# Kernel tuning notes

Hardware: AMD Instinct MI355X
Metric: run time of the kernel (lower is better)

The kernel has to match this reference:

```python
import jax, jax.numpy as jnp
import numpy as np
from itertools import combinations

F = 24                 # num_fields
VOCAB_PER_FIELD = 10000
D = 16                 # embed_dim
B = 2048               # batch
FIELD_DIMS = [VOCAB_PER_FIELD] * F
TOTAL_VOCAB = sum(FIELD_DIMS)
# FeaturesEmbedding/FeaturesLinear offsets: cumulative field dims
OFFSETS = np.concatenate(([0], np.cumsum(FIELD_DIMS)[:-1])).astype(np.int64)  # (F,)
PAIRS = np.array(list(combinations(range(F), 2)), dtype=np.int64)   # (276, 2)
TRIPS = np.array(list(combinations(range(F), 3)), dtype=np.int64)   # (2024, 3)


def setup_inputs() -> dict:
    key = jax.random.key(0)
    k0, k1, k2, k3, k4 = jax.random.split(key, 5)
    x = jax.random.randint(k0, (B, F), 0, VOCAB_PER_FIELD)
    embed_table = jax.random.normal(k1, (TOTAL_VOCAB, D), dtype=jnp.float32) * 0.01
    lin_weight = jax.random.normal(k2, (TOTAL_VOCAB, 1), dtype=jnp.float32) * 0.01
    lin_bias = jnp.zeros((1,), dtype=jnp.float32)
    genotype_2nd = jax.random.normal(k3, (PAIRS.shape[0], 1), dtype=jnp.float32)
    genotype_3rd = jax.random.normal(k4, (TRIPS.shape[0], 1), dtype=jnp.float32)
    return {
        "x": x,
        "embed_table": embed_table,
        "lin_weight": lin_weight,
        "lin_bias": lin_bias,
        "genotype_2nd": genotype_2nd,
        "genotype_3rd": genotype_3rd,
    }


def reference(x, embed_table, lin_weight, lin_bias, genotype_2nd, genotype_3rd):
    idx = x + jnp.asarray(OFFSETS)[None, :]            # (B, F) global ids
    emb = embed_table[idx]                             # (B, F, D)
    # genotype is detached in the original forward
    g2 = jax.lax.stop_gradient(genotype_2nd)[:, 0]     # (P,)
    g3 = jax.lax.stop_gradient(genotype_3rd)[:, 0]     # (T,)
    # 2nd-order gated interactions: sum_t sum_d g2[t] * e_i * e_j
    p = emb[:, PAIRS[:, 0]]                            # (B, P, D)
    q = emb[:, PAIRS[:, 1]]
    nasfm_2nd = jnp.einsum('bpd,bpd,p->b', p, q, g2)   # (B,)
    # 3rd-order gated interactions
    p1 = emb[:, TRIPS[:, 0]]                           # (B, T, D)
    q1 = emb[:, TRIPS[:, 1]]
    r1 = emb[:, TRIPS[:, 2]]
    nasfm_3rd = jnp.einsum('btd,btd,btd,t->b', p1, q1, r1, g3)  # (B,)
    # FeaturesLinear: sum of per-feature weights + bias
    linear = jnp.sum(lin_weight[idx][..., 0], axis=1) + lin_bias[0]  # (B,)
    return jax.nn.sigmoid(linear + nasfm_2nd + nasfm_3rd)
```

## Files before the change

### kernel.cpp

```cpp
#include <hip/hip_runtime.h>
#include <math.h>

#define F 24
#define D 16
#define BATCH 2048
#define NPAIR 276
#define NTRIP 2024
#define VOCAB 10000
#define SLAB 392
#define LONG_SLOTS 80
#define SHORT_SLOTS 224
#define LONG_F (LONG_SLOTS * 28)
#define CW_FLOATS (LONG_F + SHORT_SLOTS * 16)

__host__ __device__ constexpr int pair_base(int i) { return i * 23 - i * (i - 1) / 2; }
__host__ __device__ constexpr int trip_base(int i) {
    return NTRIP - (24 - i) * (23 - i) * (22 - i) / 6;
}
__host__ __device__ constexpr int trip_idx(int i, int j, int k) {
    return trip_base(i) + (j - i - 1) * (46 - i - j) / 2 + (k - j - 1);
}

__global__ void repack_kernel(const float* __restrict__ g2,
                              const float* __restrict__ g3,
                              float* __restrict__ cw) {
    const int tid = threadIdx.x;
    for (int t = tid; t < CW_FLOATS; t += 512) cw[t] = 0.f;
    __syncthreads();
    if (tid < NPAIR) {
        const int p = tid;
        int i = 0;
        while (pair_base(i + 1) <= p) ++i;
        const int j = i + 1 + (p - pair_base(i));
        if (j <= 11) {
            const int rank = i * 11 - i * (i - 1) / 2 + (j - i - 1);
            float* o = cw + rank * 28;
            o[0] = __int_as_float(i); o[1] = __int_as_float(j); o[2] = g2[p];
            for (int k = j + 1; k < F; ++k) o[4 + k] = g3[trip_idx(i, j, k)];
        } else {
            const int rank = (i <= 11) ? (12 * i + (j - 12))
                                       : (144 + (35 - i) * (i - 12) / 2 + (j - i - 1));
            float* o = cw + LONG_F + rank * 16;
            o[0] = __int_as_float(i); o[1] = __int_as_float(j); o[2] = g2[p];
            for (int k = j + 1; k < F; ++k) o[k - 10] = g3[trip_idx(i, j, k)];
        }
    }
}

__global__ __launch_bounds__(1024, 4) void ctr_main(
    const int* __restrict__ x, const float* __restrict__ emb,
    const float* __restrict__ lw, const float* __restrict__ lb,
    const float* __restrict__ cw, float* __restrict__ out) {
    __shared__ float s_e[4 * SLAB];
    __shared__ int   s_idx[4 * F];
    __shared__ float s_lw[4 * F];
    __shared__ float s_part[16][4];

    const int tid = threadIdx.x;
    const int row0 = blockIdx.x * 4;

    if (tid < 4 * F) {
        int r = tid / F, f = tid - r * F;
        int idx = x[(row0 + r) * F + f] + f * VOCAB;
        s_idx[tid] = idx;
        s_lw[tid] = lw[idx];
    }
    __syncthreads();

    if (tid < 4 * F * 4) {
        int seg = tid >> 2, q = tid & 3;
        int r = seg / F, f = seg - r * F;
        float4 v = reinterpret_cast<const float4*>(emb)[s_idx[seg] * 4 + q];
        float* b = &s_e[r * SLAB + f * D + q * 4];
        b[0] = v.x; b[1] = v.y; b[2] = v.z; b[3] = v.w;
    }
    __syncthreads();

    const int d = tid & 15;
    const int r = (tid >> 4) & 3;
    const int w = __builtin_amdgcn_readfirstlane(tid >> 6);
    const float* se = &s_e[r * SLAB];

    float e[F];
#pragma unroll
    for (int f = 0; f < F; ++f) e[f] = se[f * D + d];

    float acc = 0.f;

    const float4* Lp = reinterpret_cast<const float4*>(cw) + w * (5 * 7);
#pragma unroll 2
    for (int s = 0; s < 5; ++s) {
        float4 h  = Lp[s * 7 + 0];
        float4 c0 = Lp[s * 7 + 1], c1 = Lp[s * 7 + 2], c2 = Lp[s * 7 + 3];
        float4 c3 = Lp[s * 7 + 4], c4 = Lp[s * 7 + 5], c5 = Lp[s * 7 + 6];
        int i = __float_as_int(h.x), j = __float_as_int(h.y);
        float ei = se[i * D + d];
        float ej = se[j * D + d];
        float ta = h.z, tb = 0.f;
        ta = fmaf(c0.z, e[2],  ta); tb = fmaf(c0.w, e[3],  tb);
        ta = fmaf(c1.x, e[4],  ta); tb = fmaf(c1.y, e[5],  tb);
        ta = fmaf(c1.z, e[6],  ta); tb = fmaf(c1.w, e[7],  tb);
        ta = fmaf(c2.x, e[8],  ta); tb = fmaf(c2.y, e[9],  tb);
        ta = fmaf(c2.z, e[10], ta); tb = fmaf(c2.w, e[11], tb);
        ta = fmaf(c3.x, e[12], ta); tb = fmaf(c3.y, e[13], tb);
        ta = fmaf(c3.z, e[14], ta); tb = fmaf(c3.w, e[15], tb);
        ta = fmaf(c4.x, e[16], ta); tb = fmaf(c4.y, e[17], tb);
        ta = fmaf(c4.z, e[18], ta); tb = fmaf(c4.w, e[19], tb);
        ta = fmaf(c5.x, e[20], ta); tb = fmaf(c5.y, e[21], tb);
        ta = fmaf(c5.z, e[22], ta); tb = fmaf(c5.w, e[23], tb);
        acc = fmaf(ei * ej, ta + tb, acc);
    }

    const float4* Sp = reinterpret_cast<const float4*>(cw) + (LONG_F / 4) + w * (14 * 4);
#pragma unroll 2
    for (int s = 0; s < 14; ++s) {
        float4 h  = Sp[s * 4 + 0];
        float4 k0 = Sp[s * 4 + 1], k1 = Sp[s * 4 + 2], k2 = Sp[s * 4 + 3];
        int i = __float_as_int(h.x), j = __float_as_int(h.y);
        float ei = se[i * D + d];
        float ej = se[j * D + d];
        float ta = h.z, tb = 0.f;
        ta = fmaf(h.w,  e[13], ta);
        tb = fmaf(k0.x, e[14], tb); ta = fmaf(k0.y, e[15], ta);
        tb = fmaf(k0.z, e[16], tb); ta = fmaf(k0.w, e[17], ta);
        tb = fmaf(k1.x, e[18], tb); ta = fmaf(k1.y, e[19], ta);
        tb = fmaf(k1.z, e[20], tb); ta = fmaf(k1.w, e[21], ta);
        tb = fmaf(k2.x, e[22], tb); ta = fmaf(k2.y, e[23], ta);
        acc = fmaf(ei * ej, ta + tb, acc);
    }

#pragma unroll
    for (int m = 1; m < 16; m <<= 1) acc += __shfl_xor(acc, m, 64);
    if (d == 0) s_part[w][r] = acc;
    __syncthreads();

    if (tid < 64) {
        const int rr = tid >> 4, c = tid & 15;
        float v = s_part[c][rr];
#pragma unroll
        for (int m = 1; m < 16; m <<= 1) v += __shfl_xor(v, m, 64);
        if (c == 0) {
            float lin = lb[0];
#pragma unroll
            for (int f = 0; f < F; ++f) lin += s_lw[rr * F + f];
            float z = v + lin;
            out[row0 + rr] = 1.f / (1.f + __expf(-z));
        }
    }
}

extern "C" void kernel_launch(void* const* d_in, const int* in_sizes, int n_in,
                              void* d_out, int out_size, void* d_ws, size_t ws_size,
                              hipStream_t stream) {
    const int*   x   = (const int*)d_in[0];
    const float* emb = (const float*)d_in[1];
    const float* lw  = (const float*)d_in[2];
    const float* lb  = (const float*)d_in[3];
    const float* g2  = (const float*)d_in[4];
    const float* g3  = (const float*)d_in[5];
    float* out = (float*)d_out;
    float* cw  = (float*)d_ws;

    hipLaunchKernelGGL(repack_kernel, dim3(1), dim3(512), 0, stream, g2, g3, cw);
    hipLaunchKernelGGL(ctr_main, dim3(BATCH / 4), dim3(1024), 0, stream,
                       x, emb, lw, lb, cw, out);
}
```

Measured before the change: 19.74 us.

## Parallelize repack per output float and overlap index and embedding gathers

The gate repack kernel moves from one 512-thread block, which zeroed the buffer, synchronized, then ran serial per-pair loops, to a grid of 256-thread blocks where each thread computes exactly one output float. In the main kernel, the embedding gather threads now read x and form the global index themselves, and a separate group of threads loads the linear weights at the same time. This removes one __syncthreads and a dependent global-load round trip. The cost is that x is read redundantly, four times per embedding segment plus once more for the linear weights.

Result: faster. 17.16 us, median of 2 (-13.1%).

```diff
diff --git a/kernel.cpp b/kernel.cpp
--- a/kernel.cpp
+++ b/kernel.cpp
@@ -20,31 +20,46 @@
 __host__ __device__ constexpr int trip_idx(int i, int j, int k) {
     return trip_base(i) + (j - i - 1) * (46 - i - j) / 2 + (k - j - 1);
 }
+__device__ __forceinline__ int lbase(int i) { return 11 * i - i * (i - 1) / 2; }
+__device__ __forceinline__ int sbase(int i) { return 144 + (35 - i) * (i - 12) / 2; }
 
-__global__ void repack_kernel(const float* __restrict__ g2,
-                              const float* __restrict__ g3,
-                              float* __restrict__ cw) {
-    const int tid = threadIdx.x;
-    for (int t = tid; t < CW_FLOATS; t += 512) cw[t] = 0.f;
-    __syncthreads();
-    if (tid < NPAIR) {
-        const int p = tid;
-        int i = 0;
-        while (pair_base(i + 1) <= p) ++i;
-        const int j = i + 1 + (p - pair_base(i));
-        if (j <= 11) {
-            const int rank = i * 11 - i * (i - 1) / 2 + (j - i - 1);
-            float* o = cw + rank * 28;
-            o[0] = __int_as_float(i); o[1] = __int_as_float(j); o[2] = g2[p];
-            for (int k = j + 1; k < F; ++k) o[4 + k] = g3[trip_idx(i, j, k)];
-        } else {
-            const int rank = (i <= 11) ? (12 * i + (j - 12))
-                                       : (144 + (35 - i) * (i - 12) / 2 + (j - i - 1));
-            float* o = cw + LONG_F + rank * 16;
-            o[0] = __int_as_float(i); o[1] = __int_as_float(j); o[2] = g2[p];
-            for (int k = j + 1; k < F; ++k) o[k - 10] = g3[trip_idx(i, j, k)];
+__global__ __launch_bounds__(256) void repack_kernel(const float* __restrict__ g2,
+                                                     const float* __restrict__ g3,
+                                                     float* __restrict__ cw) {
+    const int t = blockIdx.x * 256 + threadIdx.x;
+    if (t >= CW_FLOATS) return;
+    float v = 0.f;
+    if (t < LONG_F) {
+        const int slot = t / 28, field = t - slot * 28;
+        if (slot < 66) {
+            int i = 0;
+            while (lbase(i + 1) <= slot) ++i;
+            const int j = i + 1 + (slot - lbase(i));
+            if (field == 0) v = __int_as_float(i);
+            else if (field == 1) v = __int_as_float(j);
+            else if (field == 2) v = g2[pair_base(i) + (j - i - 1)];
+            else if (field >= 4) {
+                const int k = field - 4;
+                if (k > j) v = g3[trip_idx(i, j, k)];
+            }
+        }
+    } else {
+        const int tt = t - LONG_F;
+        const int slot = tt / 16, field = tt - slot * 16;
+        if (slot < 210) {
+            int i, j;
+            if (slot < 144) { i = slot / 12; j = 12 + (slot - 12 * i); }
+            else { i = 12; while (sbase(i + 1) <= slot) ++i; j = i + 1 + (slot - sbase(i)); }
+            if (field == 0) v = __int_as_float(i);
+            else if (field == 1) v = __int_as_float(j);
+            else if (field == 2) v = g2[pair_base(i) + (j - i - 1)];
+            else if (field >= 3 && field <= 13) {
+                const int k = 10 + field;
+                if (k > j) v = g3[trip_idx(i, j, k)];
+            }
         }
     }
+    cw[t] = v;
 }
 
 __global__ __launch_bounds__(1024, 4) void ctr_main(
@@ -52,27 +67,23 @@
     const float* __restrict__ lw, const float* __restrict__ lb,
     const float* __restrict__ cw, float* __restrict__ out) {
     __shared__ float s_e[4 * SLAB];
-    __shared__ int   s_idx[4 * F];
     __shared__ float s_lw[4 * F];
     __shared__ float s_part[16][4];
 
     const int tid = threadIdx.x;
     const int row0 = blockIdx.x * 4;
 
-    if (tid < 4 * F) {
-        int r = tid / F, f = tid - r * F;
-        int idx = x[(row0 + r) * F + f] + f * VOCAB;
-        s_idx[tid] = idx;
-        s_lw[tid] = lw[idx];
-    }
-    __syncthreads();
-
     if (tid < 4 * F * 4) {
-        int seg = tid >> 2, q = tid & 3;
-        int r = seg / F, f = seg - r * F;
-        float4 v = reinterpret_cast<const float4*>(emb)[s_idx[seg] * 4 + q];
+        const int seg = tid >> 2, q = tid & 3;
+        const int r = seg / F, f = seg - r * F;
+        const int idx = x[(row0 + r) * F + f] + f * VOCAB;
+        float4 v = reinterpret_cast<const float4*>(emb)[idx * 4 + q];
         float* b = &s_e[r * SLAB + f * D + q * 4];
         b[0] = v.x; b[1] = v.y; b[2] = v.z; b[3] = v.w;
+    } else if (tid < 4 * F * 4 + 4 * F) {
+        const int tt = tid - 4 * F * 4;
+        const int r = tt / F, f = tt - r * F;
+        s_lw[tt] = lw[x[(row0 + r) * F + f] + f * VOCAB];
     }
     __syncthreads();
 
@@ -161,7 +172,8 @@
     float* out = (float*)d_out;
     float* cw  = (float*)d_ws;
 
-    hipLaunchKernelGGL(repack_kernel, dim3(1), dim3(512), 0, stream, g2, g3, cw);
+    hipLaunchKernelGGL(repack_kernel, dim3((CW_FLOATS + 255) / 256), dim3(256), 0, stream,
+                       g2, g3, cw);
     hipLaunchKernelGGL(ctr_main, dim3(BATCH / 4), dim3(1024), 0, stream,
                        x, emb, lw, lb, cw, out);
 }
```
